# Kernel optimization log

Hardware: AMD Instinct MI355X
Metric: run time of the kernel (lower is better)

## Reference

```python
import jax, jax.numpy as jnp
import numpy as np

IN_FEATURES = 2048
OUT_FEATURES = 2048
ORDER = 8
BATCH = 8192


def setup_inputs() -> dict:
    key = jax.random.key(0)
    k1, k2, k3, k4 = jax.random.split(key, 4)
    x = jax.random.normal(k1, (BATCH, IN_FEATURES), dtype=jnp.float32)
    v = jax.random.normal(k2, (ORDER, max(IN_FEATURES, OUT_FEATURES)), dtype=jnp.float32)
    d = jax.random.normal(k3, (min(IN_FEATURES, OUT_FEATURES),), dtype=jnp.float32)
    bias = jax.random.normal(k4, (OUT_FEATURES,), dtype=jnp.float32) * 0.01
    return {"x": x, "v": v, "d": d, "bias": bias}


def reference(x, v, d, bias):
    # Normalize each reflection vector (row-wise L2 norm), as in the torch module.
    n = v.shape[1]  # max_feature = 2048
    vn = v / jnp.linalg.norm(v, axis=1, keepdims=True)
    # Householder matrices H_i = I - 2 v_i v_i^T, shape [order, n, n]
    H = jnp.eye(n, dtype=x.dtype)[None, :, :] - 2.0 * jnp.einsum('ab,ac->abc', vn, vn)
    # Chain multiply u = H_0 @ H_1 @ ... @ H_{order-1} (order is a small static constant)
    u = H[0]
    for i in range(1, H.shape[0]):
        u = u @ H[i]
    # out_features <= in_features branch: W = u @ (eye(in, out) @ diag(d))
    # eye(in, out) @ diag(d) places d on the leading diagonal of an [in, out] matrix,
    # so W = u[:, :out] * d (column scaling) -- same math, no dense diag matmul.
    W = u[:, :OUT_FEATURES] * d[None, :]
    y = x @ W + bias[None, :]
    return y
```

## Files before the change

kernel.cpp:

```cpp
#include <hip/hip_runtime.h>

#define N_FEAT 2048
#define ORDER 8
#define BATCH 8192
#define BLOCK 256

__global__ __launch_bounds__(BLOCK) void normalize_v_kernel(
    const float* __restrict__ v, float* __restrict__ vn) {
    const int row = blockIdx.x;
    const int tid = threadIdx.x;
    const float* vr = v + (size_t)row * N_FEAT;

    float ss = 0.f;
    #pragma unroll
    for (int k = tid; k < N_FEAT; k += BLOCK) {
        float a = vr[k];
        ss += a * a;
    }
    #pragma unroll
    for (int o = 32; o > 0; o >>= 1) ss += __shfl_down(ss, o, 64);
    __shared__ float red[4];
    const int lane = tid & 63, wid = tid >> 6;
    if (lane == 0) red[wid] = ss;
    __syncthreads();
    const float tot = red[0] + red[1] + red[2] + red[3];
    const float inv = 1.0f / sqrtf(tot);
    #pragma unroll
    for (int k = tid; k < N_FEAT; k += BLOCK) {
        vn[(size_t)row * N_FEAT + k] = vr[k] * inv;
    }
}

__global__ __launch_bounds__(BLOCK) void orth_apply_kernel(
    const float* __restrict__ x, const float* __restrict__ vn,
    const float* __restrict__ d, const float* __restrict__ bias,
    float* __restrict__ y) {
    const int row = blockIdx.x;
    const int tid = threadIdx.x;
    const size_t base = (size_t)row * N_FEAT;

    float4 z0 = *(const float4*)(x + base + tid * 4);
    float4 z1 = *(const float4*)(x + base + 1024 + tid * 4);

    __shared__ float red[4];
    const int lane = tid & 63, wid = tid >> 6;

    #pragma unroll
    for (int i = 0; i < ORDER; ++i) {
        const float* vr = vn + (size_t)i * N_FEAT;
        const float4 a0 = *(const float4*)(vr + tid * 4);
        const float4 a1 = *(const float4*)(vr + 1024 + tid * 4);

        float p = z0.x * a0.x + z0.y * a0.y + z0.z * a0.z + z0.w * a0.w
                + z1.x * a1.x + z1.y * a1.y + z1.z * a1.z + z1.w * a1.w;
        #pragma unroll
        for (int o = 32; o > 0; o >>= 1) p += __shfl_down(p, o, 64);

        __syncthreads();
        if (lane == 0) red[wid] = p;
        __syncthreads();
        const float s = -2.0f * (red[0] + red[1] + red[2] + red[3]);

        z0.x += s * a0.x; z0.y += s * a0.y; z0.z += s * a0.z; z0.w += s * a0.w;
        z1.x += s * a1.x; z1.y += s * a1.y; z1.z += s * a1.z; z1.w += s * a1.w;
    }

    const float4 d0 = *(const float4*)(d + tid * 4);
    const float4 d1 = *(const float4*)(d + 1024 + tid * 4);
    const float4 b0 = *(const float4*)(bias + tid * 4);
    const float4 b1 = *(const float4*)(bias + 1024 + tid * 4);

    float4 o0, o1;
    o0.x = z0.x * d0.x + b0.x; o0.y = z0.y * d0.y + b0.y;
    o0.z = z0.z * d0.z + b0.z; o0.w = z0.w * d0.w + b0.w;
    o1.x = z1.x * d1.x + b1.x; o1.y = z1.y * d1.y + b1.y;
    o1.z = z1.z * d1.z + b1.z; o1.w = z1.w * d1.w + b1.w;

    *(float4*)(y + base + tid * 4) = o0;
    *(float4*)(y + base + 1024 + tid * 4) = o1;
}

extern "C" void kernel_launch(void* const* d_in, const int* in_sizes, int n_in,
                              void* d_out, int out_size, void* d_ws, size_t ws_size,
                              hipStream_t stream) {
    const float* x    = (const float*)d_in[0];
    const float* v    = (const float*)d_in[1];
    const float* d    = (const float*)d_in[2];
    const float* bias = (const float*)d_in[3];
    float* y = (float*)d_out;
    float* vn = (float*)d_ws;

    normalize_v_kernel<<<ORDER, BLOCK, 0, stream>>>(v, vn);
    orth_apply_kernel<<<BATCH, BLOCK, 0, stream>>>(x, vn, d, bias, y);
}
```

Measured before the change: 137.3 us.

## Use compact WY form to apply Householder chain with one reduction

Adds a single-block kernel that computes the Gram matrix of the normalized reflection vectors and builds the triangular T factor of the compact WY representation. The apply kernel then computes all eight dot products at once, does one block reduction, and updates each row with a small triangular combination. This replaces eight sequential reduce-and-sync rounds per row with a single one. The cost is an extra tiny kernel launch, more live registers for the eight reflection vectors, and slightly different floating-point rounding.

```diff
diff --git a/kernel.cpp b/kernel.cpp
--- a/kernel.cpp
+++ b/kernel.cpp
@@ -4,6 +4,10 @@
 #define ORDER 8
 #define BATCH 8192
 #define BLOCK 256
+
+__device__ __forceinline__ float dot4(float4 a, float4 b) {
+    return a.x * b.x + a.y * b.y + a.z * b.z + a.w * b.w;
+}
 
 __global__ __launch_bounds__(BLOCK) void normalize_v_kernel(
     const float* __restrict__ v, float* __restrict__ vn) {
@@ -23,46 +27,124 @@
     const int lane = tid & 63, wid = tid >> 6;
     if (lane == 0) red[wid] = ss;
     __syncthreads();
-    const float tot = red[0] + red[1] + red[2] + red[3];
-    const float inv = 1.0f / sqrtf(tot);
+    const float inv = 1.0f / sqrtf(red[0] + red[1] + red[2] + red[3]);
     #pragma unroll
     for (int k = tid; k < N_FEAT; k += BLOCK) {
         vn[(size_t)row * N_FEAT + k] = vr[k] * inv;
     }
 }
 
+__global__ __launch_bounds__(BLOCK) void gram_t_kernel(
+    const float* __restrict__ vn, float* __restrict__ Tout) {
+    const int tid = threadIdx.x;
+    const int lane = tid & 63, wid = tid >> 6;
+
+    float4 a0[ORDER], a1[ORDER];
+    #pragma unroll
+    for (int i = 0; i < ORDER; ++i) {
+        a0[i] = *(const float4*)(vn + (size_t)i * N_FEAT + tid * 4);
+        a1[i] = *(const float4*)(vn + (size_t)i * N_FEAT + 1024 + tid * 4);
+    }
+    float acc[28];
+    #pragma unroll
+    for (int i = 0, c = 0; i < ORDER; ++i)
+        #pragma unroll
+        for (int j = i + 1; j < ORDER; ++j, ++c)
+            acc[c] = dot4(a0[i], a0[j]) + dot4(a1[i], a1[j]);
+    #pragma unroll
+    for (int o = 32; o > 0; o >>= 1)
+        #pragma unroll
+        for (int c = 0; c < 28; ++c) acc[c] += __shfl_down(acc[c], o, 64);
+
+    __shared__ float gred[4][28];
+    if (lane == 0) {
+        #pragma unroll
+        for (int c = 0; c < 28; ++c) gred[wid][c] = acc[c];
+    }
+    __syncthreads();
+    if (tid == 0) {
+        float G[ORDER][ORDER];
+        for (int i = 0, c = 0; i < ORDER; ++i) {
+            G[i][i] = 1.0f;
+            for (int j = i + 1; j < ORDER; ++j, ++c) {
+                float g = gred[0][c] + gred[1][c] + gred[2][c] + gred[3][c];
+                G[i][j] = g; G[j][i] = g;
+            }
+        }
+        float T[ORDER][ORDER];
+        for (int i = 0; i < ORDER; ++i)
+            for (int j = 0; j < ORDER; ++j) T[i][j] = 0.f;
+        T[0][0] = 2.0f;
+        for (int k = 1; k < ORDER; ++k) {
+            for (int j = 0; j < k; ++j) {
+                float s = 0.f;
+                for (int m = j; m < k; ++m) s += T[j][m] * G[m][k];
+                T[j][k] = -2.0f * s;
+            }
+            T[k][k] = 2.0f;
+        }
+        for (int i = 0; i < ORDER; ++i)
+            for (int j = 0; j < ORDER; ++j) Tout[i * ORDER + j] = T[i][j];
+    }
+}
+
 __global__ __launch_bounds__(BLOCK) void orth_apply_kernel(
     const float* __restrict__ x, const float* __restrict__ vn,
-    const float* __restrict__ d, const float* __restrict__ bias,
-    float* __restrict__ y) {
+    const float* __restrict__ T, const float* __restrict__ d,
+    const float* __restrict__ bias, float* __restrict__ y) {
     const int row = blockIdx.x;
     const int tid = threadIdx.x;
+    const int lane = tid & 63, wid = tid >> 6;
     const size_t base = (size_t)row * N_FEAT;
 
     float4 z0 = *(const float4*)(x + base + tid * 4);
     float4 z1 = *(const float4*)(x + base + 1024 + tid * 4);
 
-    __shared__ float red[4];
-    const int lane = tid & 63, wid = tid >> 6;
+    float4 a0[ORDER], a1[ORDER];
+    #pragma unroll
+    for (int i = 0; i < ORDER; ++i) {
+        a0[i] = *(const float4*)(vn + (size_t)i * N_FEAT + tid * 4);
+        a1[i] = *(const float4*)(vn + (size_t)i * N_FEAT + 1024 + tid * 4);
+    }
+
+    float p[ORDER];
+    #pragma unroll
+    for (int i = 0; i < ORDER; ++i)
+        p[i] = dot4(z0, a0[i]) + dot4(z1, a1[i]);
+    #pragma unroll
+    for (int o = 32; o > 0; o >>= 1)
+        #pragma unroll
+        for (int i = 0; i < ORDER; ++i) p[i] += __shfl_down(p[i], o, 64);
+
+    __shared__ float red[4][ORDER];
+    __shared__ float tlds[ORDER * ORDER];
+    if (tid < ORDER * ORDER) tlds[tid] = T[tid];
+    if (lane == 0) {
+        #pragma unroll
+        for (int i = 0; i < ORDER; ++i) red[wid][i] = p[i];
+    }
+    __syncthreads();
+
+    float pp[ORDER];
+    #pragma unroll
+    for (int i = 0; i < ORDER; ++i)
+        pp[i] = red[0][i] + red[1][i] + red[2][i] + red[3][i];
+
+    float q[ORDER];
+    #pragma unroll
+    for (int j = 0; j < ORDER; ++j) {
+        float s = 0.f;
+        #pragma unroll
+        for (int i = 0; i <= j; ++i) s += pp[i] * tlds[i * ORDER + j];
+        q[j] = -s;
+    }
 
     #pragma unroll
-    for (int i = 0; i < ORDER; ++i) {
-        const float* vr = vn + (size_t)i * N_FEAT;
-        const float4 a0 = *(const float4*)(vr + tid * 4);
-        const float4 a1 = *(const float4*)(vr + 1024 + tid * 4);
-
-        float p = z0.x * a0.x + z0.y * a0.y + z0.z * a0.z + z0.w * a0.w
-                + z1.x * a1.x + z1.y * a1.y + z1.z * a1.z + z1.w * a1.w;
-        #pragma unroll
-        for (int o = 32; o > 0; o >>= 1) p += __shfl_down(p, o, 64);
-
-        __syncthreads();
-        if (lane == 0) red[wid] = p;
-        __syncthreads();
-        const float s = -2.0f * (red[0] + red[1] + red[2] + red[3]);
-
-        z0.x += s * a0.x; z0.y += s * a0.y; z0.z += s * a0.z; z0.w += s * a0.w;
-        z1.x += s * a1.x; z1.y += s * a1.y; z1.z += s * a1.z; z1.w += s * a1.w;
+    for (int j = 0; j < ORDER; ++j) {
+        z0.x += q[j] * a0[j].x; z0.y += q[j] * a0[j].y;
+        z0.z += q[j] * a0[j].z; z0.w += q[j] * a0[j].w;
+        z1.x += q[j] * a1[j].x; z1.y += q[j] * a1[j].y;
+        z1.z += q[j] * a1[j].z; z1.w += q[j] * a1[j].w;
     }
 
     const float4 d0 = *(const float4*)(d + tid * 4);
@@ -87,9 +169,11 @@
     const float* v    = (const float*)d_in[1];
     const float* d    = (const float*)d_in[2];
     const float* bias = (const float*)d_in[3];
-    float* y = (float*)d_out;
+    float* y  = (float*)d_out;
     float* vn = (float*)d_ws;
+    float* T  = vn + ORDER * N_FEAT;
 
     normalize_v_kernel<<<ORDER, BLOCK, 0, stream>>>(v, vn);
-    orth_apply_kernel<<<BATCH, BLOCK, 0, stream>>>(x, vn, d, bias, y);
+    gram_t_kernel<<<1, BLOCK, 0, stream>>>(vn, T);
+    orth_apply_kernel<<<BATCH, BLOCK, 0, stream>>>(x, vn, T, d, bias, y);
 }
```

Result: slower. 151.2 us (+10.1%).

## Process four rows per block with double-buffered reductions and nontemporal stores

Applied to the files above, without the earlier changes.

The apply kernel now handles four batch rows per block, so each Householder vector load and each block barrier is shared by four rows. A double-buffered shared reduction array removes one of the two barriers per reflection. Output writes use nontemporal stores, and the normalization becomes a single block that handles all eight vectors with batched shuffles. In exchange the grid has fewer blocks and each thread holds more registers.

```diff
diff --git a/kernel.cpp b/kernel.cpp
--- a/kernel.cpp
+++ b/kernel.cpp
@@ -4,30 +4,45 @@
 #define ORDER 8
 #define BATCH 8192
 #define BLOCK 256
+#define ROWS 4
 
-__global__ __launch_bounds__(BLOCK) void normalize_v_kernel(
+typedef float v4f __attribute__((ext_vector_type(4)));
+
+__device__ __forceinline__ float dot4(v4f a, v4f b) {
+    return a.x * b.x + a.y * b.y + a.z * b.z + a.w * b.w;
+}
+
+__global__ __launch_bounds__(BLOCK) void prep_kernel(
     const float* __restrict__ v, float* __restrict__ vn) {
-    const int row = blockIdx.x;
     const int tid = threadIdx.x;
-    const float* vr = v + (size_t)row * N_FEAT;
+    const int lane = tid & 63, wid = tid >> 6;
 
-    float ss = 0.f;
+    v4f a0[ORDER], a1[ORDER];
     #pragma unroll
-    for (int k = tid; k < N_FEAT; k += BLOCK) {
-        float a = vr[k];
-        ss += a * a;
+    for (int i = 0; i < ORDER; ++i) {
+        a0[i] = *(const v4f*)(v + (size_t)i * N_FEAT + tid * 4);
+        a1[i] = *(const v4f*)(v + (size_t)i * N_FEAT + 1024 + tid * 4);
     }
+    float ss[ORDER];
     #pragma unroll
-    for (int o = 32; o > 0; o >>= 1) ss += __shfl_down(ss, o, 64);
-    __shared__ float red[4];
-    const int lane = tid & 63, wid = tid >> 6;
-    if (lane == 0) red[wid] = ss;
+    for (int i = 0; i < ORDER; ++i)
+        ss[i] = dot4(a0[i], a0[i]) + dot4(a1[i], a1[i]);
+    #pragma unroll
+    for (int o = 32; o > 0; o >>= 1)
+        #pragma unroll
+        for (int i = 0; i < ORDER; ++i) ss[i] += __shfl_down(ss[i], o, 64);
+
+    __shared__ float red[4][ORDER];
+    if (lane == 0) {
+        #pragma unroll
+        for (int i = 0; i < ORDER; ++i) red[wid][i] = ss[i];
+    }
     __syncthreads();
-    const float tot = red[0] + red[1] + red[2] + red[3];
-    const float inv = 1.0f / sqrtf(tot);
     #pragma unroll
-    for (int k = tid; k < N_FEAT; k += BLOCK) {
-        vn[(size_t)row * N_FEAT + k] = vr[k] * inv;
+    for (int i = 0; i < ORDER; ++i) {
+        const float inv = 1.0f / sqrtf(red[0][i] + red[1][i] + red[2][i] + red[3][i]);
+        *(v4f*)(vn + (size_t)i * N_FEAT + tid * 4) = a0[i] * inv;
+        *(v4f*)(vn + (size_t)i * N_FEAT + 1024 + tid * 4) = a1[i] * inv;
     }
 }
 
@@ -35,49 +50,64 @@
     const float* __restrict__ x, const float* __restrict__ vn,
     const float* __restrict__ d, const float* __restrict__ bias,
     float* __restrict__ y) {
-    const int row = blockIdx.x;
     const int tid = threadIdx.x;
-    const size_t base = (size_t)row * N_FEAT;
+    const int lane = tid & 63, wid = tid >> 6;
+    const size_t base = (size_t)blockIdx.x * ROWS * N_FEAT;
+    const int c0 = tid * 4;
+    const int c1 = 1024 + tid * 4;
 
-    float4 z0 = *(const float4*)(x + base + tid * 4);
-    float4 z1 = *(const float4*)(x + base + 1024 + tid * 4);
+    v4f z0[ROWS], z1[ROWS];
+    #pragma unroll
+    for (int r = 0; r < ROWS; ++r) {
+        z0[r] = *(const v4f*)(x + base + (size_t)r * N_FEAT + c0);
+        z1[r] = *(const v4f*)(x + base + (size_t)r * N_FEAT + c1);
+    }
 
-    __shared__ float red[4];
-    const int lane = tid & 63, wid = tid >> 6;
+    __shared__ float red[2][4][ROWS];
 
     #pragma unroll
     for (int i = 0; i < ORDER; ++i) {
         const float* vr = vn + (size_t)i * N_FEAT;
-        const float4 a0 = *(const float4*)(vr + tid * 4);
-        const float4 a1 = *(const float4*)(vr + 1024 + tid * 4);
+        const v4f a0 = *(const v4f*)(vr + c0);
+        const v4f a1 = *(const v4f*)(vr + c1);
 
-        float p = z0.x * a0.x + z0.y * a0.y + z0.z * a0.z + z0.w * a0.w
-                + z1.x * a1.x + z1.y * a1.y + z1.z * a1.z + z1.w * a1.w;
+        float p[ROWS];
         #pragma unroll
-        for (int o = 32; o > 0; o >>= 1) p += __shfl_down(p, o, 64);
+        for (int r = 0; r < ROWS; ++r)
+            p[r] = dot4(z0[r], a0) + dot4(z1[r], a1);
+        #pragma unroll
+        for (int o = 32; o > 0; o >>= 1)
+            #pragma unroll
+            for (int r = 0; r < ROWS; ++r) p[r] += __shfl_down(p[r], o, 64);
 
+        const int buf = i & 1;
+        if (lane == 0) {
+            #pragma unroll
+            for (int r = 0; r < ROWS; ++r) red[buf][wid][r] = p[r];
+        }
         __syncthreads();
-        if (lane == 0) red[wid] = p;
-        __syncthreads();
-        const float s = -2.0f * (red[0] + red[1] + red[2] + red[3]);
 
-        z0.x += s * a0.x; z0.y += s * a0.y; z0.z += s * a0.z; z0.w += s * a0.w;
-        z1.x += s * a1.x; z1.y += s * a1.y; z1.z += s * a1.z; z1.w += s * a1.w;
+        #pragma unroll
+        for (int r = 0; r < ROWS; ++r) {
+            const float s = -2.0f * (red[buf][0][r] + red[buf][1][r] +
+                                     red[buf][2][r] + red[buf][3][r]);
+            z0[r] += s * a0;
+            z1[r] += s * a1;
+        }
     }
 
-    const float4 d0 = *(const float4*)(d + tid * 4);
-    const float4 d1 = *(const float4*)(d + 1024 + tid * 4);
-    const float4 b0 = *(const float4*)(bias + tid * 4);
-    const float4 b1 = *(const float4*)(bias + 1024 + tid * 4);
+    const v4f d0 = *(const v4f*)(d + c0);
+    const v4f d1 = *(const v4f*)(d + c1);
+    const v4f b0 = *(const v4f*)(bias + c0);
+    const v4f b1 = *(const v4f*)(bias + c1);
 
-    float4 o0, o1;
-    o0.x = z0.x * d0.x + b0.x; o0.y = z0.y * d0.y + b0.y;
-    o0.z = z0.z * d0.z + b0.z; o0.w = z0.w * d0.w + b0.w;
-    o1.x = z1.x * d1.x + b1.x; o1.y = z1.y * d1.y + b1.y;
-    o1.z = z1.z * d1.z + b1.z; o1.w = z1.w * d1.w + b1.w;
-
-    *(float4*)(y + base + tid * 4) = o0;
-    *(float4*)(y + base + 1024 + tid * 4) = o1;
+    #pragma unroll
+    for (int r = 0; r < ROWS; ++r) {
+        v4f o0 = z0[r] * d0 + b0;
+        v4f o1 = z1[r] * d1 + b1;
+        __builtin_nontemporal_store(o0, (v4f*)(y + base + (size_t)r * N_FEAT + c0));
+        __builtin_nontemporal_store(o1, (v4f*)(y + base + (size_t)r * N_FEAT + c1));
+    }
 }
 
 extern "C" void kernel_launch(void* const* d_in, const int* in_sizes, int n_in,
@@ -87,9 +117,9 @@
     const float* v    = (const float*)d_in[1];
     const float* d    = (const float*)d_in[2];
     const float* bias = (const float*)d_in[3];
-    float* y = (float*)d_out;
+    float* y  = (float*)d_out;
     float* vn = (float*)d_ws;
 
-    normalize_v_kernel<<<ORDER, BLOCK, 0, stream>>>(v, vn);
-    orth_apply_kernel<<<BATCH, BLOCK, 0, stream>>>(x, vn, d, bias, y);
+    prep_kernel<<<1, BLOCK, 0, stream>>>(v, vn);
+    orth_apply_kernel<<<BATCH / ROWS, BLOCK, 0, stream>>>(x, vn, d, bias, y);
 }
```

After: 126.1 us. 1.09x faster.
